# Optimization experiments

Measured on AMD Instinct MI355X. Metric: run time of the kernel, lower is better.

## Reference

```python
import jax, jax.numpy as jnp
import numpy as np

B, E, S, D = 32, 64, 50, 300   # batch, sentences/essay, words/sentence, word dim
F = 100                        # conv filters (cnn_lstm_convunits_size)
H = 100                        # lstm units (cnn_lstm_att_pool_size)
W_WIN = 5                      # word window length


def setup_inputs() -> dict:
    key = jax.random.key(0)
    ks = jax.random.split(key, 12)
    n = lambda k, shape: (jax.random.normal(k, shape, jnp.float32) * 0.05)
    return {
        "essays": jax.random.normal(ks[0], (B, E, S, D), jnp.float32),
        "conv_k": n(ks[1], (1, W_WIN, D, F)),      # HWIO
        "conv_b": jnp.zeros((F,), jnp.float32),
        "att1_mat": n(ks[2], (F, F)),
        "att1_bias": n(ks[3], (F,)),
        "att1_vec": n(ks[4], (F, 1)),
        "lstm_W": n(ks[5], (F + H, 4 * H)),        # TF BasicLSTMCell kernel, gate order i,j,f,o
        "lstm_b": jnp.zeros((4 * H,), jnp.float32),
        "att2_mat": n(ks[6], (H, H)),
        "att2_bias": n(ks[7], (H,)),
        "att2_vec": n(ks[8], (H, 1)),
        "dense_w": n(ks[9], (H, 1)),
        "dense_b": jnp.zeros((1,), jnp.float32),
    }


def reference(essays, conv_k, conv_b, att1_mat, att1_bias, att1_vec,
              lstm_W, lstm_b, att2_mat, att2_bias, att2_vec,
              dense_w, dense_b):
    # conv2d, kernel [1, w_window_len], SAME padding, relu  -> [B,E,S,F]
    conv1 = jax.lax.conv_general_dilated(
        essays, conv_k, window_strides=(1, 1), padding="SAME",
        dimension_numbers=("NHWC", "HWIO", "NHWC"))
    conv1 = jax.nn.relu(conv1 + conv_b)

    # attention pooling over words (axis=2)
    a1 = jnp.tanh(jnp.einsum("besf,fg->besg", conv1, att1_mat) + att1_bias)
    a1 = jnp.einsum("besg,go->beso", a1, att1_vec)          # [B,E,S,1]
    a1 = jax.nn.softmax(a1, axis=2)
    sent = jnp.sum(a1 * conv1, axis=2)                       # [B,E,F]

    # BasicLSTMCell (forget_bias=1.0, gate order i,j,f,o) over sentence axis
    hdim = lstm_b.shape[0] // 4
    bsz = essays.shape[0]

    def step(carry, xt):
        c, h = carry
        z = jnp.concatenate([xt, h], axis=1) @ lstm_W + lstm_b
        i, j, f, o = jnp.split(z, 4, axis=1)
        c = c * jax.nn.sigmoid(f + 1.0) + jax.nn.sigmoid(i) * jnp.tanh(j)
        h = jax.nn.sigmoid(o) * jnp.tanh(c)
        return (c, h), h

    init = (jnp.zeros((bsz, hdim), sent.dtype), jnp.zeros((bsz, hdim), sent.dtype))
    xs = jnp.swapaxes(sent, 0, 1)                            # [E,B,F]
    _, hs = jax.lax.scan(step, init, xs)
    lstm = jnp.swapaxes(hs, 0, 1)                            # [B,E,H]

    # attention pooling over sentences (axis=1)
    a2 = jnp.tanh(jnp.einsum("beh,hg->beg", lstm, att2_mat) + att2_bias)
    a2 = jnp.einsum("beg,go->beo", a2, att2_vec)             # [B,E,1]
    a2 = jax.nn.softmax(a2, axis=1)
    essay_repr = jnp.sum(a2 * lstm, axis=1)                  # [B,H]

    preds = jax.nn.sigmoid(essay_repr @ dense_w + dense_b).reshape(-1)  # [B]
    return preds
```

## Files before the change

kernel.cpp:

```cpp
#include <hip/hip_runtime.h>
#include <hip/hip_bf16.h>
#include <stdint.h>

#define Bsz 32
#define Esz 64
#define Ssz 50
#define Dsz 300
#define Fsz 100
#define Hsz 100
#define WWIN 5

#define PX   328
#define PC   136
#define KT_CONV 50
#define NTILES  7
#define MTILES  4
#define NGRP 2214

typedef __attribute__((ext_vector_type(8))) short bf16x8;
typedef __attribute__((ext_vector_type(8))) unsigned short u16x8;
typedef __attribute__((ext_vector_type(4))) float f32x4;

__device__ __forceinline__ float sigmoid_fast(float x) {
    return 1.0f / (1.0f + __expf(-x));
}
__device__ __forceinline__ float tanhf_fast(float x) {
    const float ax = fabsf(x);
    const float e = __expf(2.0f * ax);
    const float t = 1.0f - 2.0f / (e + 1.0f);
    return copysignf(t, x);
}

__device__ __forceinline__ unsigned short f2bf(float x) {
    union { __hip_bfloat16 h; unsigned short u; } cv;
    cv.h = __float2bfloat16(x);
    return cv.u;
}
__device__ __forceinline__ unsigned int f2bf2(float lo, float hi) {
    union { __hip_bfloat162 h2; unsigned int u; } cv;
    cv.h2 = __float22bfloat162_rn(make_float2(lo, hi));
    return cv.u;
}
__device__ __forceinline__ float bf2f(unsigned short b) {
    union { uint32_t u; float f; } v; v.u = ((uint32_t)b) << 16;
    return v.f;
}

#define N_BTGC (KT_CONV * 112 * 32)
#define N_BTGA (4 * 112 * 32)
#define N_BTGW (4 * 400 * 32)

__global__ __launch_bounds__(256) void prep_kernel(
    const float* __restrict__ conv_k, const float* __restrict__ att1_mat,
    const float* __restrict__ lstm_W,
    unsigned short* __restrict__ BtgC, unsigned short* __restrict__ BtgA,
    unsigned short* __restrict__ BtgW)
{
    const int total = N_BTGC + N_BTGA + N_BTGW;
    for (int i = blockIdx.x * 256 + threadIdx.x; i < total; i += gridDim.x * 256) {
        if (i < N_BTGC) {
            const int kt = i / (112 * 32);
            const int r  = i % (112 * 32);
            const int n  = r / 32;
            const int kk = r % 32;
            const int w  = kt / 10;
            const int d  = (kt % 10) * 32 + kk;
            float val = (d < Dsz && n < Fsz) ? conv_k[((size_t)w * Dsz + d) * Fsz + n] : 0.f;
            BtgC[i] = f2bf(val);
        } else if (i < N_BTGC + N_BTGA) {
            const int j  = i - N_BTGC;
            const int kt = j / (112 * 32);
            const int r  = j % (112 * 32);
            const int n  = r / 32;
            const int kk = r % 32;
            const int k  = kt * 32 + kk;
            float val = (k < Fsz && n < Fsz) ? att1_mat[(size_t)k * Fsz + n] : 0.f;
            BtgA[j] = f2bf(val);
        } else {
            const int j  = i - N_BTGC - N_BTGA;
            const int kt = j / (400 * 32);
            const int r  = j % (400 * 32);
            const int n  = r / 32;
            const int kk = r % 32;
            const int k  = kt * 32 + kk;
            float val = (k < Fsz) ? lstm_W[(size_t)k * 400 + n] : 0.f;
            BtgW[j] = f2bf(val);
        }
    }
}

template<int G>
__device__ __forceinline__ void conv_loadB(
    const unsigned short* __restrict__ BtgC, int boff0, int boff1, bool has1,
    bf16x8 (&bR)[5][2])
{
#pragma unroll
    for (int i = 0; i < 5; ++i) {
        const int kt = G * 5 + i;
        bR[i][0] = *reinterpret_cast<const bf16x8*>(BtgC + kt * 3584 + boff0);
        bR[i][1] = has1 ? *reinterpret_cast<const bf16x8*>(BtgC + kt * 3584 + boff1)
                        : (bf16x8)0;
    }
}

template<int KT>
__device__ __forceinline__ void conv_loadA(
    const unsigned short* b0p, const unsigned short* b1p,
    const int (&abase)[MTILES], bf16x8 (&a)[2][MTILES])
{
    constexpr int w   = KT / 10;
    constexpr int t   = KT % 10;
    constexpr int off = w * PX + t * 32;
#pragma unroll
    for (int mt = 0; mt < MTILES; ++mt) {
        a[0][mt] = *reinterpret_cast<const bf16x8*>(&b0p[abase[mt] + off]);
        a[1][mt] = *reinterpret_cast<const bf16x8*>(&b1p[abase[mt] + off]);
    }
}

__device__ __forceinline__ void mfma16(
    const bf16x8 (&a)[2][MTILES], const bf16x8 (&b)[2], bool has1,
    f32x4 (&acc)[2][MTILES][2])
{
    __builtin_amdgcn_s_setprio(1);
#pragma unroll
    for (int es = 0; es < 2; ++es) {
#pragma unroll
        for (int mt = 0; mt < MTILES; ++mt) {
            acc[es][mt][0] = __builtin_amdgcn_mfma_f32_16x16x32_bf16(a[es][mt], b[0], acc[es][mt][0], 0, 0, 0);
            if (has1)
                acc[es][mt][1] = __builtin_amdgcn_mfma_f32_16x16x32_bf16(a[es][mt], b[1], acc[es][mt][1], 0, 0, 0);
        }
    }
    __builtin_amdgcn_s_setprio(0);
}

template<int KT>
__device__ __forceinline__ void conv_kt(
    const unsigned short* b0p, const unsigned short* b1p,
    const int (&abase)[MTILES], bool has1, const bf16x8 (&b)[2],
    bf16x8 (&aX)[2][MTILES], bf16x8 (&aY)[2][MTILES],
    f32x4 (&acc)[2][MTILES][2])
{
    constexpr bool even = (KT % 2) == 0;
    if constexpr (KT + 1 < KT_CONV) {
        if constexpr (even) conv_loadA<KT + 1>(b0p, b1p, abase, aY);
        else                conv_loadA<KT + 1>(b0p, b1p, abase, aX);
    }
    if constexpr (even) mfma16(aX, b, has1, acc);
    else                mfma16(aY, b, has1, acc);
}

template<int G>
__device__ __forceinline__ void conv_group(
    const unsigned short* b0p, const unsigned short* b1p,
    const int (&abase)[MTILES], bool has1, const bf16x8 (&bR)[5][2],
    bf16x8 (&aX)[2][MTILES], bf16x8 (&aY)[2][MTILES],
    f32x4 (&acc)[2][MTILES][2])
{
    conv_kt<G * 5 + 0>(b0p, b1p, abase, has1, bR[0], aX, aY, acc);
    conv_kt<G * 5 + 1>(b0p, b1p, abase, has1, bR[1], aX, aY, acc);
    conv_kt<G * 5 + 2>(b0p, b1p, abase, has1, bR[2], aX, aY, acc);
    conv_kt<G * 5 + 3>(b0p, b1p, abase, has1, bR[3], aX, aY, acc);
    conv_kt<G * 5 + 4>(b0p, b1p, abase, has1, bR[4], aX, aY, acc);
}

template<int KT>
__device__ __forceinline__ void att_loadA(
    const unsigned short* b0p, const unsigned short* b1p,
    const int (&abase2)[MTILES], bf16x8 (&a)[2][MTILES])
{
    constexpr int off = KT * 32;
#pragma unroll
    for (int mt = 0; mt < MTILES; ++mt) {
        a[0][mt] = *reinterpret_cast<const bf16x8*>(&b0p[abase2[mt] + off]);
        a[1][mt] = *reinterpret_cast<const bf16x8*>(&b1p[abase2[mt] + off]);
    }
}

__global__ __launch_bounds__(256, 2) void conv_att1_kernel(
    const float* __restrict__ essays,
    const unsigned short* __restrict__ BtgC,
    const unsigned short* __restrict__ BtgA,
    const float* __restrict__ conv_b,
    const float* __restrict__ att1_bias,
    const float* __restrict__ att1_vec,
    unsigned short* __restrict__ sent_bf)
{
    __shared__ __align__(16) unsigned short buf[2][54 * PX];
    __shared__ float u_s[2][64];
    __shared__ float alpha_s[2][64];

    const int be0 = blockIdx.x * 2;
    const int tid = threadIdx.x;
    const int lane = tid & 63;
    const int wid  = tid >> 6;
    const int ln   = lane & 15;
    const int qd   = lane >> 4;

    if (tid < 128) u_s[tid >> 6][tid & 63] = 0.f;

    const int nt0 = wid;
    const int nt1 = wid + 4;
    const bool has1 = (nt1 < NTILES);
    const int boff0 = (nt0 * 16 + ln) * 32 + 8 * qd;
    const int boff1 = (nt1 * 16 + ln) * 32 + 8 * qd;

    int abase[MTILES];
#pragma unroll
    for (int mt = 0; mt < MTILES; ++mt) {
        const int m = mt * 16 + ln;
        abase[mt] = (m < Ssz ? m : Ssz - 1) * PX + 8 * qd;
    }

    bf16x8 bX[5][2], bY[5][2];
    conv_loadB<0>(BtgC, boff0, boff1, has1, bX);
    conv_loadB<1>(BtgC, boff0, boff1, has1, bY);

#pragma unroll
    for (int es = 0; es < 2; ++es) {
        const float* in_g = essays + (size_t)(be0 + es) * (Ssz * Dsz);
        float4 va[9], vb[9];
        int rr[9], cc[9];
        bool hv[9], fv[9], gv[9];
#pragma unroll
        for (int it = 0; it < 9; ++it) {
            const int g  = tid + it * 256;
            const int r  = g / 41;
            const int c8 = (g - r * 41) * 8;
            const int s  = r - 2;
            gv[it] = (g < NGRP);
            hv[it] = gv[it] && (s >= 0) && (s < Ssz) && (c8 < Dsz);
            fv[it] = hv[it] && (c8 + 8 <= Dsz);
            const float* base = in_g + (hv[it] ? (s * Dsz + c8) : 0);
            va[it] = *reinterpret_cast<const float4*>(base);
            vb[it] = *reinterpret_cast<const float4*>(fv[it] ? base + 4 : base);
            rr[it] = r; cc[it] = c8;
        }
#pragma unroll
        for (int it = 0; it < 9; ++it) {
            if (!gv[it]) continue;
            const float e0 = hv[it] ? va[it].x : 0.f;
            const float e1 = hv[it] ? va[it].y : 0.f;
            const float e2 = hv[it] ? va[it].z : 0.f;
            const float e3 = hv[it] ? va[it].w : 0.f;
            const float e4 = fv[it] ? vb[it].x : 0.f;
            const float e5 = fv[it] ? vb[it].y : 0.f;
            const float e6 = fv[it] ? vb[it].z : 0.f;
            const float e7 = fv[it] ? vb[it].w : 0.f;
            uint4 o;
            o.x = f2bf2(e0, e1);
            o.y = f2bf2(e2, e3);
            o.z = f2bf2(e4, e5);
            o.w = f2bf2(e6, e7);
            *reinterpret_cast<uint4*>(&buf[es][rr[it] * PX + cc[it]]) = o;
        }
    }
    __syncthreads();

    const unsigned short* b0p = buf[0];
    const unsigned short* b1p = buf[1];

    f32x4 acc[2][MTILES][2];
#pragma unroll
    for (int es = 0; es < 2; ++es)
#pragma unroll
        for (int mt = 0; mt < MTILES; ++mt) { acc[es][mt][0] = (f32x4)0.f; acc[es][mt][1] = (f32x4)0.f; }

    {
        bf16x8 aX[2][MTILES], aY[2][MTILES];
        conv_loadA<0>(b0p, b1p, abase, aX);
        conv_group<0>(b0p, b1p, abase, has1, bX, aX, aY, acc);
        conv_loadB<2>(BtgC, boff0, boff1, has1, bX);
        conv_group<1>(b0p, b1p, abase, has1, bY, aX, aY, acc);
        conv_loadB<3>(BtgC, boff0, boff1, has1, bY);
        conv_group<2>(b0p, b1p, abase, has1, bX, aX, aY, acc);
        conv_loadB<4>(BtgC, boff0, boff1, has1, bX);
        conv_group<3>(b0p, b1p, abase, has1, bY, aX, aY, acc);
        conv_loadB<5>(BtgC, boff0, boff1, has1, bY);
        conv_group<4>(b0p, b1p, abase, has1, bX, aX, aY, acc);
        conv_loadB<6>(BtgC, boff0, boff1, has1, bX);
        conv_group<5>(b0p, b1p, abase, has1, bY, aX, aY, acc);
        conv_loadB<7>(BtgC, boff0, boff1, has1, bY);
        conv_group<6>(b0p, b1p, abase, has1, bX, aX, aY, acc);
        conv_loadB<8>(BtgC, boff0, boff1, has1, bX);
        conv_group<7>(b0p, b1p, abase, has1, bY, aX, aY, acc);
        conv_loadB<9>(BtgC, boff0, boff1, has1, bY);
        conv_group<8>(b0p, b1p, abase, has1, bX, aX, aY, acc);
        conv_group<9>(b0p, b1p, abase, has1, bY, aX, aY, acc);
    }

    bf16x8 a1b[4][2];
#pragma unroll
    for (int kt = 0; kt < 4; ++kt) {
        a1b[kt][0] = *reinterpret_cast<const bf16x8*>(BtgA + kt * 3584 + boff0);
        a1b[kt][1] = has1 ? *reinterpret_cast<const bf16x8*>(BtgA + kt * 3584 + boff1)
                          : (bf16x8)0;
    }
    __syncthreads();

    {
        const float bias0 = conv_b[nt0 * 16 + ln];
        const int n_g1 = nt1 * 16 + ln;
        const bool g1ok = has1 && (n_g1 < Fsz);
        const float bias1 = g1ok ? conv_b[n_g1] : 0.f;
#pragma unroll
        for (int es = 0; es < 2; ++es) {
#pragma unroll
            for (int mt = 0; mt < MTILES; ++mt) {
#pragma unroll
                for (int j = 0; j < 4; ++j) {
                    const int m_row = mt * 16 + qd * 4 + j;
                    buf[es][m_row * PC + nt0 * 16 + ln] = f2bf(fmaxf(acc[es][mt][0][j] + bias0, 0.f));
                    if (g1ok)
                        buf[es][m_row * PC + n_g1] = f2bf(fmaxf(acc[es][mt][1][j] + bias1, 0.f));
                }
            }
        }
    }
    for (int idx = tid; idx < 2 * 64 * 2; idx += 256) {
        const int es = idx >> 7;
        const int r2 = idx & 127;
        const int row = r2 >> 1;
        const int c = 112 + (r2 & 1) * 8;
        *reinterpret_cast<u16x8*>(&buf[es][row * PC + c]) = (u16x8)0;
    }
    __syncthreads();

    f32x4 acc2[2][MTILES][2];
#pragma unroll
    for (int es = 0; es < 2; ++es)
#pragma unroll
        for (int mt = 0; mt < MTILES; ++mt) { acc2[es][mt][0] = (f32x4)0.f; acc2[es][mt][1] = (f32x4)0.f; }

    {
        int abase2[MTILES];
#pragma unroll
        for (int mt = 0; mt < MTILES; ++mt) abase2[mt] = (mt * 16 + ln) * PC + 8 * qd;

        bf16x8 aX[2][MTILES], aY[2][MTILES];
        att_loadA<0>(b0p, b1p, abase2, aX);
        att_loadA<1>(b0p, b1p, abase2, aY);
        mfma16(aX, a1b[0], has1, acc2);
        att_loadA<2>(b0p, b1p, abase2, aX);
        mfma16(aY, a1b[1], has1, acc2);
        att_loadA<3>(b0p, b1p, abase2, aY);
        mfma16(aX, a1b[2], has1, acc2);
        mfma16(aY, a1b[3], has1, acc2);
    }

    {
        const int g0 = nt0 * 16 + ln;
        const float b1v0 = att1_bias[g0];
        const float vv0  = att1_vec[g0];
        const int g1 = nt1 * 16 + ln;
        const bool g1v = has1 && (g1 < Fsz);
        const float b1v1 = g1v ? att1_bias[g1] : 0.f;
        const float vv1  = g1v ? att1_vec[g1]  : 0.f;
#pragma unroll
        for (int es = 0; es < 2; ++es) {
#pragma unroll
            for (int mt = 0; mt < MTILES; ++mt) {
#pragma unroll
                for (int j = 0; j < 4; ++j) {
                    const int m_row = mt * 16 + qd * 4 + j;
                    float val = 0.f;
                    if (m_row < Ssz) {
                        val = tanhf_fast(acc2[es][mt][0][j] + b1v0) * vv0;
                        if (g1v) val += tanhf_fast(acc2[es][mt][1][j] + b1v1) * vv1;
                    }
                    val += __shfl_xor(val, 1);
                    val += __shfl_xor(val, 2);
                    val += __shfl_xor(val, 4);
                    val += __shfl_xor(val, 8);
                    if (ln == 0 && m_row < Ssz) atomicAdd(&u_s[es][m_row], val);
                }
            }
        }
    }
    __syncthreads();

    if (wid < 2) {
        const float uv = (lane < Ssz) ? u_s[wid][lane] : -1e30f;
        float m = uv;
#pragma unroll
        for (int off = 32; off > 0; off >>= 1) m = fmaxf(m, __shfl_xor(m, off));
        float e = (lane < Ssz) ? __expf(uv - m) : 0.f;
        float sum = e;
#pragma unroll
        for (int off = 32; off > 0; off >>= 1) sum += __shfl_xor(sum, off);
        alpha_s[wid][lane] = e / sum;
    }
    __syncthreads();

    {
        const int es = tid >> 7;
        const int f  = tid & 127;
        unsigned short v = 0;
        if (f < Fsz) {
            float a = 0.f;
            for (int s = 0; s < Ssz; ++s) a += alpha_s[es][s] * bf2f(buf[es][s * PC + f]);
            v = f2bf(a);
        }
        sent_bf[(size_t)(be0 + es) * 128 + f] = v;
    }
}

__global__ __launch_bounds__(256) void xpart_kernel(
    const unsigned short* __restrict__ sent_bf,
    const unsigned short* __restrict__ BtgW,
    const float* __restrict__ lstm_b,
    float* __restrict__ xpartB)
{
    const int wid  = threadIdx.x >> 6;
    const int mt   = blockIdx.x * 4 + wid;
    const int lane = threadIdx.x & 63;
    const int ln   = lane & 15;
    const int qd   = lane >> 4;
    const int m0   = mt * 16;

    f32x4 acc[25];
#pragma unroll
    for (int nt = 0; nt < 25; ++nt) acc[nt] = (f32x4)0.f;

#pragma unroll
    for (int kt = 0; kt < 4; ++kt) {
        const bf16x8 a = *reinterpret_cast<const bf16x8*>(
            sent_bf + (size_t)(m0 + ln) * 128 + kt * 32 + 8 * qd);
#pragma unroll
        for (int nt = 0; nt < 25; ++nt) {
            const bf16x8 b = *reinterpret_cast<const bf16x8*>(
                BtgW + ((size_t)kt * 400 + nt * 16 + ln) * 32 + 8 * qd);
            acc[nt] = __builtin_amdgcn_mfma_f32_16x16x32_bf16(a, b, acc[nt], 0, 0, 0);
        }
    }

#pragma unroll
    for (int nt = 0; nt < 25; ++nt) {
        const int col = nt * 16 + ln;
        const int gate = col / 100;
        const int cell = col - gate * 100;
        const float bias = lstm_b[col];
        const int gi = cell * 4 + gate;
#pragma unroll
        for (int j = 0; j < 4; ++j) {
            const int row = m0 + qd * 4 + j;
            xpartB[(size_t)row * 400 + gi] = acc[nt][j] + bias;
        }
    }
}

__global__ __launch_bounds__(448) void lstm_att2_kernel(
    const float* __restrict__ xpartB,
    const float* __restrict__ lstm_W,
    const float* __restrict__ att2_mat,
    const float* __restrict__ att2_bias,
    const float* __restrict__ att2_vec,
    const float* __restrict__ dense_w,
    const float* __restrict__ dense_b,
    float* __restrict__ out)
{
    __shared__ __align__(16) float xp_lds[Esz * 400];
    __shared__ __align__(16) float hist[Esz * Hsz];
    __shared__ __align__(16) float h_lds[2][Hsz];
    __shared__ float u2_s[Esz];
    __shared__ float alpha2_s[Esz];
    __shared__ float repr_s[Hsz];

    const int b   = blockIdx.x;
    const int tid = threadIdx.x;
    const int lane = tid & 63;
    const bool actv = tid < 400;
    const int cell = tid >> 2;
    const int g    = tid & 3;
    const int qbase = lane & 60;

    {
        const float4* src = reinterpret_cast<const float4*>(xpartB + (size_t)b * Esz * 400);
        float4* dst = reinterpret_cast<float4*>(xp_lds);
        for (int i = tid; i < Esz * 100; i += 448) dst[i] = src[i];
    }

    float w[100];
    if (actv) {
        const int col = g * 100 + cell;
#pragma unroll
        for (int k = 0; k < 100; ++k) w[k] = lstm_W[(size_t)(Fsz + k) * 400 + col];
    }
    if (tid < Hsz) h_lds[0][tid] = 0.f;
    float c = 0.f;
    __syncthreads();

    for (int t = 0; t < Esz; ++t) {
        float z = 0.f;
        if (actv) {
            const float4* h4 = reinterpret_cast<const float4*>(h_lds[t & 1]);
            float z0 = xp_lds[t * 400 + tid], z1 = 0.f, z2 = 0.f, z3 = 0.f;
#pragma unroll
            for (int k4 = 0; k4 < 25; ++k4) {
                const float4 hv = h4[k4];
                z0 += hv.x * w[4 * k4 + 0];
                z1 += hv.y * w[4 * k4 + 1];
                z2 += hv.z * w[4 * k4 + 2];
                z3 += hv.w * w[4 * k4 + 3];
            }
            z = (z0 + z1) + (z2 + z3);
        }
        const float zi = __shfl(z, qbase + 0);
        const float zj = __shfl(z, qbase + 1);
        const float zf = __shfl(z, qbase + 2);
        const float zo = __shfl(z, qbase + 3);
        if (actv) {
            c = c * sigmoid_fast(zf + 1.0f) + sigmoid_fast(zi) * tanhf_fast(zj);
            const float h = sigmoid_fast(zo) * tanhf_fast(c);
            if (g == 0) {
                h_lds[(t + 1) & 1][cell] = h;
                hist[t * Hsz + cell] = h;
            }
        }
        __syncthreads();
    }

    float* w2_s = xp_lds;
    for (int idx = tid; idx < Esz * Hsz; idx += 448) {
        const int e = idx / Hsz;
        const int gg = idx - e * Hsz;
        const float* lp = hist + e * Hsz;
        float a0 = 0.f, a1 = 0.f, a2 = 0.f, a3 = 0.f;
        for (int k = 0; k < Hsz; k += 4) {
            a0 += lp[k + 0] * att2_mat[(k + 0) * Hsz + gg];
            a1 += lp[k + 1] * att2_mat[(k + 1) * Hsz + gg];
            a2 += lp[k + 2] * att2_mat[(k + 2) * Hsz + gg];
            a3 += lp[k + 3] * att2_mat[(k + 3) * Hsz + gg];
        }
        w2_s[idx] = tanhf_fast(att2_bias[gg] + ((a0 + a1) + (a2 + a3))) * att2_vec[gg];
    }
    __syncthreads();

    if (tid < Esz) {
        float acc = 0.f;
        const float* wp = w2_s + tid * Hsz;
        for (int gg = 0; gg < Hsz; ++gg) acc += wp[gg];
        u2_s[tid] = acc;
    }
    __syncthreads();

    if (tid < 64) {
        const float uv = u2_s[tid];
        float m = uv;
#pragma unroll
        for (int off = 32; off > 0; off >>= 1) m = fmaxf(m, __shfl_xor(m, off));
        float e = __expf(uv - m);
        float sum = e;
#pragma unroll
        for (int off = 32; off > 0; off >>= 1) sum += __shfl_xor(sum, off);
        alpha2_s[tid] = e / sum;
    }
    __syncthreads();

    if (tid < Hsz) {
        float acc = 0.f;
        for (int e = 0; e < Esz; ++e) acc += alpha2_s[e] * hist[e * Hsz + tid];
        repr_s[tid] = acc;
    }
    __syncthreads();

    if (tid == 0) {
        float acc = dense_b[0];
        for (int hh = 0; hh < Hsz; ++hh) acc += repr_s[hh] * dense_w[hh];
        out[b] = sigmoid_fast(acc);
    }
}

extern "C" void kernel_launch(void* const* d_in, const int* in_sizes, int n_in,
                              void* d_out, int out_size, void* d_ws, size_t ws_size,
                              hipStream_t stream) {
    const float* essays    = (const float*)d_in[0];
    const float* conv_k    = (const float*)d_in[1];
    const float* conv_b    = (const float*)d_in[2];
    const float* att1_mat  = (const float*)d_in[3];
    const float* att1_bias = (const float*)d_in[4];
    const float* att1_vec  = (const float*)d_in[5];
    const float* lstm_W    = (const float*)d_in[6];
    const float* lstm_b    = (const float*)d_in[7];
    const float* att2_mat  = (const float*)d_in[8];
    const float* att2_bias = (const float*)d_in[9];
    const float* att2_vec  = (const float*)d_in[10];
    const float* dense_w   = (const float*)d_in[11];
    const float* dense_b   = (const float*)d_in[12];

    float* out = (float*)d_out;

    char* ws = (char*)d_ws;
    unsigned short* sent_bf = (unsigned short*)ws;
    float* xpartB = (float*)(ws + 524288);
    unsigned short* BtgC = (unsigned short*)(ws + 3801088);
    unsigned short* BtgA = (unsigned short*)(ws + 4159488);
    unsigned short* BtgW = (unsigned short*)(ws + 4188160);

    prep_kernel<<<512, 256, 0, stream>>>(conv_k, att1_mat, lstm_W, BtgC, BtgA, BtgW);
    conv_att1_kernel<<<Bsz * Esz / 2, 256, 0, stream>>>(
        essays, BtgC, BtgA, conv_b, att1_bias, att1_vec, sent_bf);
    xpart_kernel<<<32, 256, 0, stream>>>(sent_bf, BtgW, lstm_b, xpartB);
    lstm_att2_kernel<<<Bsz, 448, 0, stream>>>(
        xpartB, lstm_W, att2_mat, att2_bias, att2_vec, dense_w, dense_b, out);
}
```

Before: 207.9 us.

## Use fp16 packed dot products and DPP gate broadcast in LSTM recurrence

The LSTM recurrent matvec now keeps weights packed as fp16 pairs in registers, prepared by the prep kernel in a gate-interleaved layout. The hidden state is stored in LDS as fp16, and each step uses fdot2, halving both the register footprint and the LDS reads. Gate values are broadcast within each quad using DPP moves instead of ds_bpermute shuffles, shortening the serial per-step critical path. The cost is reduced precision in the recurrent term.

```diff
diff --git a/kernel.cpp b/kernel.cpp
--- a/kernel.cpp
+++ b/kernel.cpp
@@ -20,6 +20,10 @@
 typedef __attribute__((ext_vector_type(8))) short bf16x8;
 typedef __attribute__((ext_vector_type(8))) unsigned short u16x8;
 typedef __attribute__((ext_vector_type(4))) float f32x4;
+typedef _Float16 half2_t __attribute__((ext_vector_type(2)));
+
+union UH32 { unsigned int u; half2_t v; };
+union UH16 { _Float16 h; unsigned short u; };
 
 __device__ __forceinline__ float sigmoid_fast(float x) {
     return 1.0f / (1.0f + __expf(-x));
@@ -45,18 +49,29 @@
     union { uint32_t u; float f; } v; v.u = ((uint32_t)b) << 16;
     return v.f;
 }
+__device__ __forceinline__ float dpp_bcast(float z, const int sel) {
+    int r;
+    switch (sel) {
+        case 0: r = __builtin_amdgcn_mov_dpp(__builtin_bit_cast(int, z), 0x00, 0xf, 0xf, false); break;
+        case 1: r = __builtin_amdgcn_mov_dpp(__builtin_bit_cast(int, z), 0x55, 0xf, 0xf, false); break;
+        case 2: r = __builtin_amdgcn_mov_dpp(__builtin_bit_cast(int, z), 0xaa, 0xf, 0xf, false); break;
+        default: r = __builtin_amdgcn_mov_dpp(__builtin_bit_cast(int, z), 0xff, 0xf, 0xf, false); break;
+    }
+    return __builtin_bit_cast(float, r);
+}
 
 #define N_BTGC (KT_CONV * 112 * 32)
 #define N_BTGA (4 * 112 * 32)
 #define N_BTGW (4 * 400 * 32)
+#define N_BTGP (52 * 400)
 
 __global__ __launch_bounds__(256) void prep_kernel(
     const float* __restrict__ conv_k, const float* __restrict__ att1_mat,
     const float* __restrict__ lstm_W,
     unsigned short* __restrict__ BtgC, unsigned short* __restrict__ BtgA,
-    unsigned short* __restrict__ BtgW)
-{
-    const int total = N_BTGC + N_BTGA + N_BTGW;
+    unsigned short* __restrict__ BtgW, unsigned int* __restrict__ BtgP)
+{
+    const int total = N_BTGC + N_BTGA + N_BTGW + N_BTGP;
     for (int i = blockIdx.x * 256 + threadIdx.x; i < total; i += gridDim.x * 256) {
         if (i < N_BTGC) {
             const int kt = i / (112 * 32);
@@ -76,7 +91,7 @@
             const int k  = kt * 32 + kk;
             float val = (k < Fsz && n < Fsz) ? att1_mat[(size_t)k * Fsz + n] : 0.f;
             BtgA[j] = f2bf(val);
-        } else {
+        } else if (i < N_BTGC + N_BTGA + N_BTGW) {
             const int j  = i - N_BTGC - N_BTGA;
             const int kt = j / (400 * 32);
             const int r  = j % (400 * 32);
@@ -85,6 +100,20 @@
             const int k  = kt * 32 + kk;
             float val = (k < Fsz) ? lstm_W[(size_t)k * 400 + n] : 0.f;
             BtgW[j] = f2bf(val);
+        } else {
+            const int j   = i - N_BTGC - N_BTGA - N_BTGW;
+            const int k2  = j / 400;
+            const int col = j - k2 * 400;
+            const int gate = col & 3;
+            const int cell = col >> 2;
+            const int src  = gate * 100 + cell;
+            const int k0 = 2 * k2, k1 = 2 * k2 + 1;
+            const float v0 = (k0 < Hsz) ? lstm_W[(size_t)(Fsz + k0) * 400 + src] : 0.f;
+            const float v1 = (k1 < Hsz) ? lstm_W[(size_t)(Fsz + k1) * 400 + src] : 0.f;
+            union { _Float16 h[2]; unsigned int u; } cv;
+            cv.h[0] = (_Float16)v0;
+            cv.h[1] = (_Float16)v1;
+            BtgP[j] = cv.u;
         }
     }
 }
@@ -452,7 +481,7 @@
 
 __global__ __launch_bounds__(448) void lstm_att2_kernel(
     const float* __restrict__ xpartB,
-    const float* __restrict__ lstm_W,
+    const unsigned int* __restrict__ BtgP,
     const float* __restrict__ att2_mat,
     const float* __restrict__ att2_bias,
     const float* __restrict__ att2_vec,
@@ -462,18 +491,16 @@
 {
     __shared__ __align__(16) float xp_lds[Esz * 400];
     __shared__ __align__(16) float hist[Esz * Hsz];
-    __shared__ __align__(16) float h_lds[2][Hsz];
+    __shared__ __align__(16) unsigned short h16[2][104];
     __shared__ float u2_s[Esz];
     __shared__ float alpha2_s[Esz];
     __shared__ float repr_s[Hsz];
 
     const int b   = blockIdx.x;
     const int tid = threadIdx.x;
-    const int lane = tid & 63;
     const bool actv = tid < 400;
     const int cell = tid >> 2;
     const int g    = tid & 3;
-    const int qbase = lane & 60;
 
     {
         const float4* src = reinterpret_cast<const float4*>(xpartB + (size_t)b * Esz * 400);
@@ -481,40 +508,44 @@
         for (int i = tid; i < Esz * 100; i += 448) dst[i] = src[i];
     }
 
-    float w[100];
+    unsigned int wp[52];
     if (actv) {
-        const int col = g * 100 + cell;
-#pragma unroll
-        for (int k = 0; k < 100; ++k) w[k] = lstm_W[(size_t)(Fsz + k) * 400 + col];
-    }
-    if (tid < Hsz) h_lds[0][tid] = 0.f;
+#pragma unroll
+        for (int q = 0; q < 52; ++q) wp[q] = BtgP[q * 400 + tid];
+    }
+    if (tid < 104) { h16[0][tid] = 0; h16[1][tid] = 0; }
     float c = 0.f;
     __syncthreads();
 
     for (int t = 0; t < Esz; ++t) {
         float z = 0.f;
         if (actv) {
-            const float4* h4 = reinterpret_cast<const float4*>(h_lds[t & 1]);
-            float z0 = xp_lds[t * 400 + tid], z1 = 0.f, z2 = 0.f, z3 = 0.f;
-#pragma unroll
-            for (int k4 = 0; k4 < 25; ++k4) {
-                const float4 hv = h4[k4];
-                z0 += hv.x * w[4 * k4 + 0];
-                z1 += hv.y * w[4 * k4 + 1];
-                z2 += hv.z * w[4 * k4 + 2];
-                z3 += hv.w * w[4 * k4 + 3];
+            const uint4* hq = reinterpret_cast<const uint4*>(h16[t & 1]);
+            float za = xp_lds[t * 400 + tid], zb = 0.f, zc = 0.f, zd = 0.f;
+#pragma unroll
+            for (int q = 0; q < 13; ++q) {
+                const uint4 hv = hq[q];
+                UH32 h0, h1, h2, h3, w0, w1, w2, w3;
+                h0.u = hv.x; h1.u = hv.y; h2.u = hv.z; h3.u = hv.w;
+                w0.u = wp[4 * q + 0]; w1.u = wp[4 * q + 1];
+                w2.u = wp[4 * q + 2]; w3.u = wp[4 * q + 3];
+                za = __builtin_amdgcn_fdot2(w0.v, h0.v, za, false);
+                zb = __builtin_amdgcn_fdot2(w1.v, h1.v, zb, false);
+                zc = __builtin_amdgcn_fdot2(w2.v, h2.v, zc, false);
+                zd = __builtin_amdgcn_fdot2(w3.v, h3.v, zd, false);
             }
-            z = (z0 + z1) + (z2 + z3);
-        }
-        const float zi = __shfl(z, qbase + 0);
-        const float zj = __shfl(z, qbase + 1);
-        const float zf = __shfl(z, qbase + 2);
-        const float zo = __shfl(z, qbase + 3);
-        if (actv) {
+            z = (za + zb) + (zc + zd);
+
+            const float zi = dpp_bcast(z, 0);
+            const float zj = dpp_bcast(z, 1);
+            const float zf = dpp_bcast(z, 2);
+            const float zo = dpp_bcast(z, 3);
+
             c = c * sigmoid_fast(zf + 1.0f) + sigmoid_fast(zi) * tanhf_fast(zj);
             const float h = sigmoid_fast(zo) * tanhf_fast(c);
             if (g == 0) {
-                h_lds[(t + 1) & 1][cell] = h;
+                UH16 cv; cv.h = (_Float16)h;
+                h16[(t + 1) & 1][cell] = cv.u;
                 hist[t * Hsz + cell] = h;
             }
         }
@@ -539,8 +570,8 @@
 
     if (tid < Esz) {
         float acc = 0.f;
-        const float* wp = w2_s + tid * Hsz;
-        for (int gg = 0; gg < Hsz; ++gg) acc += wp[gg];
+        const float* wpp = w2_s + tid * Hsz;
+        for (int gg = 0; gg < Hsz; ++gg) acc += wpp[gg];
         u2_s[tid] = acc;
     }
     __syncthreads();
@@ -597,11 +628,12 @@
     unsigned short* BtgC = (unsigned short*)(ws + 3801088);
     unsigned short* BtgA = (unsigned short*)(ws + 4159488);
     unsigned short* BtgW = (unsigned short*)(ws + 4188160);
-
-    prep_kernel<<<512, 256, 0, stream>>>(conv_k, att1_mat, lstm_W, BtgC, BtgA, BtgW);
+    unsigned int*   BtgP = (unsigned int*)(ws + 4290560);
+
+    prep_kernel<<<512, 256, 0, stream>>>(conv_k, att1_mat, lstm_W, BtgC, BtgA, BtgW, BtgP);
     conv_att1_kernel<<<Bsz * Esz / 2, 256, 0, stream>>>(
         essays, BtgC, BtgA, conv_b, att1_bias, att1_vec, sent_bf);
     xpart_kernel<<<32, 256, 0, stream>>>(sent_bf, BtgW, lstm_b, xpartB);
     lstm_att2_kernel<<<Bsz, 448, 0, stream>>>(
-        xpartB, lstm_W, att2_mat, att2_bias, att2_vec, dense_w, dense_b, out);
-}
+        xpartB, BtgP, att2_mat, att2_bias, att2_vec, dense_w, dense_b, out);
+}
```

New measurement: 185.9 us. 1.12x faster.

## Use fp16 dot2 with K-split across quad lanes in LSTM recurrence

Applied to the files above, without the earlier changes.

The LSTM recurrent matvec now stores recurrent weights as packed fp16 pairs, prepared in the prep kernel. Each lane of a 4-lane quad handles a quarter of the hidden dimension for all four gates of one cell, using fdot2 instructions. Partial sums are combined with DPP quad reductions instead of four cross-lane shuffles. The hidden state is kept in LDS as fp16, which cuts per-step FMA count and register pressure on the serial critical path. The cost is reduced precision in h and in the weights.

```diff
diff --git a/kernel.cpp b/kernel.cpp
--- a/kernel.cpp
+++ b/kernel.cpp
@@ -20,6 +20,10 @@
 typedef __attribute__((ext_vector_type(8))) short bf16x8;
 typedef __attribute__((ext_vector_type(8))) unsigned short u16x8;
 typedef __attribute__((ext_vector_type(4))) float f32x4;
+typedef _Float16 half2_t __attribute__((ext_vector_type(2)));
+
+union UH32 { unsigned int u; half2_t v; };
+union UH16 { _Float16 h; unsigned short u; };
 
 __device__ __forceinline__ float sigmoid_fast(float x) {
     return 1.0f / (1.0f + __expf(-x));
@@ -45,18 +49,26 @@
     union { uint32_t u; float f; } v; v.u = ((uint32_t)b) << 16;
     return v.f;
 }
+__device__ __forceinline__ float quad_ar(float x) {
+    int r = __builtin_amdgcn_mov_dpp(__builtin_bit_cast(int, x), 0xB1, 0xf, 0xf, false);
+    x += __builtin_bit_cast(float, r);
+    r = __builtin_amdgcn_mov_dpp(__builtin_bit_cast(int, x), 0x4E, 0xf, 0xf, false);
+    x += __builtin_bit_cast(float, r);
+    return x;
+}
 
 #define N_BTGC (KT_CONV * 112 * 32)
 #define N_BTGA (4 * 112 * 32)
 #define N_BTGW (4 * 400 * 32)
+#define N_BTGQ (16 * 400 * 4)
 
 __global__ __launch_bounds__(256) void prep_kernel(
     const float* __restrict__ conv_k, const float* __restrict__ att1_mat,
     const float* __restrict__ lstm_W,
     unsigned short* __restrict__ BtgC, unsigned short* __restrict__ BtgA,
-    unsigned short* __restrict__ BtgW)
-{
-    const int total = N_BTGC + N_BTGA + N_BTGW;
+    unsigned short* __restrict__ BtgW, unsigned int* __restrict__ BtgQ)
+{
+    const int total = N_BTGC + N_BTGA + N_BTGW + N_BTGQ;
     for (int i = blockIdx.x * 256 + threadIdx.x; i < total; i += gridDim.x * 256) {
         if (i < N_BTGC) {
             const int kt = i / (112 * 32);
@@ -76,7 +88,7 @@
             const int k  = kt * 32 + kk;
             float val = (k < Fsz && n < Fsz) ? att1_mat[(size_t)k * Fsz + n] : 0.f;
             BtgA[j] = f2bf(val);
-        } else {
+        } else if (i < N_BTGC + N_BTGA + N_BTGW) {
             const int j  = i - N_BTGC - N_BTGA;
             const int kt = j / (400 * 32);
             const int r  = j % (400 * 32);
@@ -85,6 +97,23 @@
             const int k  = kt * 32 + kk;
             float val = (k < Fsz) ? lstm_W[(size_t)k * 400 + n] : 0.f;
             BtgW[j] = f2bf(val);
+        } else {
+            const int j   = i - N_BTGC - N_BTGA - N_BTGW;
+            const int c   = j & 3;
+            const int r   = j >> 2;
+            const int k2q = r / 400;
+            const int tt  = r - k2q * 400;
+            const int g    = tt & 3;
+            const int cell = tt >> 2;
+            const int k0 = 32 * g + 2 * k2q;
+            const float v0 = (k0 < Hsz)
+                ? lstm_W[(size_t)(Fsz + k0) * 400 + c * 100 + cell] : 0.f;
+            const float v1 = (k0 + 1 < Hsz)
+                ? lstm_W[(size_t)(Fsz + k0 + 1) * 400 + c * 100 + cell] : 0.f;
+            union { _Float16 h[2]; unsigned int u; } cv;
+            cv.h[0] = (_Float16)v0;
+            cv.h[1] = (_Float16)v1;
+            BtgQ[j] = cv.u;
         }
     }
 }
@@ -452,7 +481,7 @@
 
 __global__ __launch_bounds__(448) void lstm_att2_kernel(
     const float* __restrict__ xpartB,
-    const float* __restrict__ lstm_W,
+    const unsigned int* __restrict__ BtgQ,
     const float* __restrict__ att2_mat,
     const float* __restrict__ att2_bias,
     const float* __restrict__ att2_vec,
@@ -462,18 +491,16 @@
 {
     __shared__ __align__(16) float xp_lds[Esz * 400];
     __shared__ __align__(16) float hist[Esz * Hsz];
-    __shared__ __align__(16) float h_lds[2][Hsz];
+    __shared__ __align__(16) unsigned short h16[2][160];
     __shared__ float u2_s[Esz];
     __shared__ float alpha2_s[Esz];
     __shared__ float repr_s[Hsz];
 
     const int b   = blockIdx.x;
     const int tid = threadIdx.x;
-    const int lane = tid & 63;
     const bool actv = tid < 400;
     const int cell = tid >> 2;
     const int g    = tid & 3;
-    const int qbase = lane & 60;
 
     {
         const float4* src = reinterpret_cast<const float4*>(xpartB + (size_t)b * Esz * 400);
@@ -481,40 +508,49 @@
         for (int i = tid; i < Esz * 100; i += 448) dst[i] = src[i];
     }
 
-    float w[100];
+    uint4 wq[16];
     if (actv) {
-        const int col = g * 100 + cell;
-#pragma unroll
-        for (int k = 0; k < 100; ++k) w[k] = lstm_W[(size_t)(Fsz + k) * 400 + col];
-    }
-    if (tid < Hsz) h_lds[0][tid] = 0.f;
-    float c = 0.f;
+#pragma unroll
+        for (int q = 0; q < 16; ++q)
+            wq[q] = *reinterpret_cast<const uint4*>(BtgQ + ((size_t)q * 400 + tid) * 4);
+    }
+    if (tid < 160) { h16[0][tid] = 0; h16[1][tid] = 0; }
+    float cstate = 0.f;
     __syncthreads();
 
     for (int t = 0; t < Esz; ++t) {
-        float z = 0.f;
         if (actv) {
-            const float4* h4 = reinterpret_cast<const float4*>(h_lds[t & 1]);
-            float z0 = xp_lds[t * 400 + tid], z1 = 0.f, z2 = 0.f, z3 = 0.f;
-#pragma unroll
-            for (int k4 = 0; k4 < 25; ++k4) {
-                const float4 hv = h4[k4];
-                z0 += hv.x * w[4 * k4 + 0];
-                z1 += hv.y * w[4 * k4 + 1];
-                z2 += hv.z * w[4 * k4 + 2];
-                z3 += hv.w * w[4 * k4 + 3];
+            const uint4* hq = reinterpret_cast<const uint4*>(&h16[t & 1][g * 40]);
+            const float4 xp4 = *reinterpret_cast<const float4*>(&xp_lds[t * 400 + cell * 4]);
+
+            float p0 = 0.f, p1 = 0.f, p2 = 0.f, p3 = 0.f;
+#pragma unroll
+            for (int j4 = 0; j4 < 4; ++j4) {
+                const uint4 hv = hq[j4];
+                const unsigned int hu0 = hv.x, hu1 = hv.y, hu2 = hv.z, hu3 = hv.w;
+#pragma unroll
+                for (int q = 0; q < 4; ++q) {
+                    UH32 hh;
+                    hh.u = (q == 0) ? hu0 : (q == 1) ? hu1 : (q == 2) ? hu2 : hu3;
+                    const uint4 wv = wq[j4 * 4 + q];
+                    UH32 w0, w1, w2, w3;
+                    w0.u = wv.x; w1.u = wv.y; w2.u = wv.z; w3.u = wv.w;
+                    p0 = __builtin_amdgcn_fdot2(w0.v, hh.v, p0, false);
+                    p1 = __builtin_amdgcn_fdot2(w1.v, hh.v, p1, false);
+                    p2 = __builtin_amdgcn_fdot2(w2.v, hh.v, p2, false);
+                    p3 = __builtin_amdgcn_fdot2(w3.v, hh.v, p3, false);
+                }
             }
-            z = (z0 + z1) + (z2 + z3);
-        }
-        const float zi = __shfl(z, qbase + 0);
-        const float zj = __shfl(z, qbase + 1);
-        const float zf = __shfl(z, qbase + 2);
-        const float zo = __shfl(z, qbase + 3);
-        if (actv) {
-            c = c * sigmoid_fast(zf + 1.0f) + sigmoid_fast(zi) * tanhf_fast(zj);
-            const float h = sigmoid_fast(zo) * tanhf_fast(c);
+            const float zi = quad_ar(p0) + xp4.x;
+            const float zj = quad_ar(p1) + xp4.y;
+            const float zf = quad_ar(p2) + xp4.z;
+            const float zo = quad_ar(p3) + xp4.w;
+
+            cstate = cstate * sigmoid_fast(zf + 1.0f) + sigmoid_fast(zi) * tanhf_fast(zj);
+            const float h = sigmoid_fast(zo) * tanhf_fast(cstate);
             if (g == 0) {
-                h_lds[(t + 1) & 1][cell] = h;
+                UH16 cv; cv.h = (_Float16)h;
+                h16[(t + 1) & 1][(cell >> 5) * 40 + (cell & 31)] = cv.u;
                 hist[t * Hsz + cell] = h;
             }
         }
@@ -539,8 +575,8 @@
 
     if (tid < Esz) {
         float acc = 0.f;
-        const float* wp = w2_s + tid * Hsz;
-        for (int gg = 0; gg < Hsz; ++gg) acc += wp[gg];
+        const float* wpp = w2_s + tid * Hsz;
+        for (int gg = 0; gg < Hsz; ++gg) acc += wpp[gg];
         u2_s[tid] = acc;
     }
     __syncthreads();
@@ -597,11 +633,12 @@
     unsigned short* BtgC = (unsigned short*)(ws + 3801088);
     unsigned short* BtgA = (unsigned short*)(ws + 4159488);
     unsigned short* BtgW = (unsigned short*)(ws + 4188160);
-
-    prep_kernel<<<512, 256, 0, stream>>>(conv_k, att1_mat, lstm_W, BtgC, BtgA, BtgW);
+    unsigned int*   BtgQ = (unsigned int*)(ws + 4290560);
+
+    prep_kernel<<<512, 256, 0, stream>>>(conv_k, att1_mat, lstm_W, BtgC, BtgA, BtgW, BtgQ);
     conv_att1_kernel<<<Bsz * Esz / 2, 256, 0, stream>>>(
         essays, BtgC, BtgA, conv_b, att1_bias, att1_vec, sent_bf);
     xpart_kernel<<<32, 256, 0, stream>>>(sent_bf, BtgW, lstm_b, xpartB);
     lstm_att2_kernel<<<Bsz, 448, 0, stream>>>(
-        xpartB, lstm_W, att2_mat, att2_bias, att2_vec, dense_w, dense_b, out);
-}
+        xpartB, BtgQ, att2_mat, att2_bias, att2_vec, dense_w, dense_b, out);
+}
```

After: 187.6 us. 9.7% less time.
